# Kernel tuning notes

Measured on AMD Instinct MI355X. Metric: run time of the kernel, lower is better.

The kernel has to match this reference:

```python
import jax, jax.numpy as jnp
import numpy as np

IN_F = 512
OUT_F = 512
ALPHA = 0.1  # leaky relu slope
NEG_INF = jnp.float32(-9e15)


def setup_inputs() -> dict:
    key = jax.random.key(0)
    k1, k2, k3, k4, k5 = jax.random.split(key, 5)
    bs, t = 16, 1024
    x_a = jax.random.normal(k1, (bs, t, IN_F), dtype=jnp.float32)
    x_v = jax.random.normal(k2, (bs, t, IN_F), dtype=jnp.float32)
    adj = jax.random.randint(k3, (bs, 2 * t, 2 * t), 0, 2, dtype=jnp.int32)
    # xavier_uniform with gain=1.414
    gain = 1.414
    limW = gain * np.sqrt(6.0 / (IN_F + OUT_F))
    W = jax.random.uniform(k4, (IN_F, OUT_F), minval=-limW, maxval=limW, dtype=jnp.float32)
    lima = gain * np.sqrt(6.0 / (2 * OUT_F + 1))
    a = jax.random.uniform(k5, (2 * OUT_F, 1), minval=-lima, maxval=lima, dtype=jnp.float32)
    return {"x_a": x_a, "x_v": x_v, "adj": adj, "W": W, "a": a}


def reference(x_a, x_v, adj, W, a):
    # h: (bs, 2t, in_f)
    h = jnp.concatenate([x_a, x_v], axis=1)
    Wh = jnp.matmul(h, W)                      # (bs, 2t, out_f)
    Wh1 = jnp.matmul(Wh, a[:OUT_F, :])         # (bs, 2t, 1)
    Wh2 = jnp.matmul(Wh, a[OUT_F:, :])         # (bs, 2t, 1)
    e = jax.nn.leaky_relu(Wh1 + jnp.swapaxes(Wh2, -1, -2), negative_slope=ALPHA)  # (bs, 2t, 2t)
    attention = jnp.where(adj > 0, e, NEG_INF)
    attention = jax.nn.softmax(attention, axis=-1)
    h_prime = jnp.matmul(attention, Wh)        # (bs, 2t, out_f)
    h_prime = jax.nn.elu(h_prime)
    t = x_a.shape[1]
    return h_prime[:, :t, :], h_prime[:, t:, :]
```

## Files before the change

### kernel.cpp

```cpp
#include <hip/hip_runtime.h>
#include <hip/hip_bf16.h>
#include <stdint.h>

typedef __attribute__((ext_vector_type(4))) float f32x4;
typedef __attribute__((ext_vector_type(8))) short short8;
typedef __attribute__((ext_vector_type(8))) unsigned short u16x8;
typedef __attribute__((ext_vector_type(4))) unsigned short u16x4;

typedef __attribute__((address_space(1))) const unsigned int as1_u32;
typedef __attribute__((address_space(3))) unsigned int as3_u32;
#define GLD16(src, dst) __builtin_amdgcn_global_load_lds((as1_u32*)(src), (as3_u32*)(dst), 16, 0, 0)

__device__ __forceinline__ unsigned short f2bf(float f) {
  unsigned int u = __float_as_uint(f);
  u += 0x7fffu + ((u >> 16) & 1u);
  return (unsigned short)(u >> 16);
}
__device__ __forceinline__ float bf2f(unsigned short h) {
  return __uint_as_float(((unsigned int)h) << 16);
}

__global__ __launch_bounds__(256) void k_twp(const float* __restrict__ W,
                                             unsigned short* __restrict__ WT) {
  __shared__ float tile[64][65];
  int tid = threadIdx.x;
  int c = tid & 63, r0 = tid >> 6;
  int kb = blockIdx.x * 64, nb = blockIdx.y * 64;
#pragma unroll
  for (int rr = 0; rr < 16; ++rr) {
    int r = rr * 4 + r0;
    tile[r][c] = W[(size_t)(kb + r) * 512 + nb + c];
  }
  __syncthreads();
#pragma unroll
  for (int rr = 0; rr < 16; ++rr) {
    int r = rr * 4 + r0;
    WT[(size_t)(nb + r) * 512 + kb + c] = f2bf(tile[c][r]);
  }
}

__global__ __launch_bounds__(256, 2) void k_gemm(const float* __restrict__ xa,
                                                 const float* __restrict__ xv,
                                                 const unsigned short* __restrict__ WT,
                                                 unsigned short* __restrict__ WhT) {
  __shared__ __align__(16) unsigned short Al[64 * 64];
  __shared__ __align__(16) unsigned short Bl[512 * 64];
  int tid = threadIdx.x;
  int rblk = blockIdx.x;
  int R0g = rblk * 64;
  int b = R0g >> 11;
  int iloc = R0g & 2047;
  const float* Abase = (iloc < 1024)
      ? (xa + ((size_t)b * 1024 + iloc) * 512)
      : (xv + ((size_t)b * 1024 + (iloc - 1024)) * 512);

  int lane = tid & 63;
  int wid = tid >> 6;
  int wc = wid;

  f32x4 acc[4][8];
#pragma unroll
  for (int i = 0; i < 4; ++i)
#pragma unroll
    for (int j = 0; j < 8; ++j) acc[i][j] = (f32x4){0.f, 0.f, 0.f, 0.f};

  for (int kt = 0; kt < 8; ++kt) {
    int k0 = kt * 64;
    __syncthreads();
#pragma unroll
    for (int pass = 0; pass < 4; ++pass) {
      int row = pass * 16 + (tid >> 4);
      int gg = tid & 15;
      float4 v = *((const float4*)(Abase + (size_t)row * 512 + k0) + gg);
      u16x4 pk;
      pk.x = f2bf(v.x); pk.y = f2bf(v.y); pk.z = f2bf(v.z); pk.w = f2bf(v.w);
      *(u16x4*)((char*)Al + row * 128 + ((gg * 8) ^ ((row & 7) << 4))) = pk;
    }
#pragma unroll
    for (int pass = 0; pass < 16; ++pass) {
      int n = pass * 32 + (tid >> 3);
      int g = tid & 7;
      const unsigned short* src = WT + (size_t)n * 512 + k0 + ((g ^ (n & 7)) << 3);
      unsigned short* dst = Bl + pass * 2048 + wid * 512;
      GLD16(src, dst);
    }
    __syncthreads();
#pragma unroll
    for (int kc = 0; kc < 2; ++kc) {
      int u = kc * 4 + (lane >> 4);
      short8 af[4];
#pragma unroll
      for (int mf = 0; mf < 4; ++mf) {
        int row = mf * 16 + (lane & 15);
        af[mf] = *(const short8*)((const char*)Al + row * 128 + (((u ^ (row & 7)) & 7) << 4));
      }
#pragma unroll
      for (int nf = 0; nf < 8; ++nf) {
        int n = wc * 128 + nf * 16 + (lane & 15);
        short8 bv = *(const short8*)((const char*)Bl + n * 128 + (((u ^ (n & 7)) & 7) << 4));
#pragma unroll
        for (int mf = 0; mf < 4; ++mf)
          acc[mf][nf] = __builtin_amdgcn_mfma_f32_16x16x32_bf16(af[mf], bv, acc[mf][nf], 0, 0, 0);
      }
    }
  }
#pragma unroll
  for (int mf = 0; mf < 4; ++mf) {
    int jrow = iloc + mf * 16 + ((lane >> 4) << 2);
#pragma unroll
    for (int nf = 0; nf < 8; ++nf) {
      int n = wc * 128 + nf * 16 + (lane & 15);
      u16x4 pk;
#pragma unroll
      for (int e = 0; e < 4; ++e) pk[e] = f2bf(acc[mf][nf][e]);
      *(u16x4*)(WhT + ((size_t)b * 512 + n) * 2048 + jrow) = pk;
    }
  }
}

__global__ __launch_bounds__(256) void k_s(const unsigned short* __restrict__ WhT,
                                           const float* __restrict__ a,
                                           float* __restrict__ s1, float* __restrict__ s2,
                                           float* __restrict__ f1, float* __restrict__ f2) {
  __shared__ float a1l[512], a2l[512];
  __shared__ float S1p[8][256], S2p[8][256];
  int tid = threadIdx.x;
  int b = blockIdx.y;
  int j0 = blockIdx.x * 256;
  a1l[tid] = a[tid]; a1l[256 + tid] = a[256 + tid];
  a2l[tid] = a[512 + tid]; a2l[256 + tid] = a[768 + tid];
  __syncthreads();
  int jv = (tid & 31) * 8;
  int nh = tid >> 5;
  const unsigned short* base = WhT + ((size_t)b * 512 + nh * 64) * 2048 + j0 + jv;
  float c1[8], c2[8];
#pragma unroll
  for (int e = 0; e < 8; ++e) { c1[e] = 0.f; c2[e] = 0.f; }
#pragma unroll 4
  for (int i = 0; i < 64; ++i) {
    u16x8 w = *(const u16x8*)(base + (size_t)i * 2048);
    float w1 = a1l[nh * 64 + i], w2 = a2l[nh * 64 + i];
#pragma unroll
    for (int e = 0; e < 8; ++e) {
      float wv = bf2f(w[e]);
      c1[e] += wv * w1;
      c2[e] += wv * w2;
    }
  }
#pragma unroll
  for (int e = 0; e < 8; ++e) { S1p[nh][jv + e] = c1[e]; S2p[nh][jv + e] = c2[e]; }
  __syncthreads();
  float v1 = 0.f, v2 = 0.f;
#pragma unroll
  for (int h = 0; h < 8; ++h) { v1 += S1p[h][tid]; v2 += S2p[h][tid]; }
  size_t o = (size_t)b * 2048 + j0 + tid;
  s1[o] = v1; s2[o] = v2;
  f1[o] = __expf(v2);
  f2[o] = __expf(0.1f * v2);
}

__global__ __launch_bounds__(512, 2) void k_attn(const int* __restrict__ adj,
                                                 const unsigned short* __restrict__ WhT,
                                                 const float* __restrict__ s1g,
                                                 const float* __restrict__ s2g,
                                                 const float* __restrict__ f1g,
                                                 const float* __restrict__ f2g,
                                                 float* __restrict__ out) {
  __shared__ __align__(16) unsigned short Bl[2 * 512 * 32];
  __shared__ __align__(16) unsigned short Pl[2 * 128 * 32];
  __shared__ float f1l[2048], f2l[2048];
  __shared__ float zl[128];
  __shared__ float red[8];
  int tid = threadIdx.x;
  int bx = blockIdx.x;
  int q = bx >> 3, xcd = bx & 7;
  int b = xcd * 2 + (q & 1);
  int rb = q >> 1;
  int R0 = rb * 128;

  int lane = tid & 63, wid = tid >> 6;
  int wr2 = wid >> 2, wc = wid & 3;
  int r = tid >> 2, qc = tid & 3;

  const unsigned short* whbase = WhT + (size_t)b * 512 * 2048;
  const int* adjrow = adj + ((size_t)b * 2048 + R0 + r) * 2048 + qc * 8;

  auto stageB = [&](int j0h, int buf) {
#pragma unroll
    for (int pass = 0; pass < 4; ++pass) {
      int n = pass * 128 + (tid >> 2);
      int g = tid & 3;
      const unsigned short* src = whbase + (size_t)n * 2048 + j0h + ((g ^ (n & 3)) << 3);
      unsigned short* dst = Bl + buf * 16384 + pass * 4096 + wid * 512;
      GLD16(src, dst);
    }
  };

  stageB(0, 0);
  int4 aL0 = *(const int4*)(adjrow + 0);
  int4 aL1 = *(const int4*)(adjrow + 4);
  int4 aH0 = *(const int4*)(adjrow + 32);
  int4 aH1 = *(const int4*)(adjrow + 36);

  float lm = -1e30f;
#pragma unroll
  for (int i = 0; i < 4; ++i) {
    int idx = i * 512 + tid;
    float v = s2g[(size_t)b * 2048 + idx];
    f1l[idx] = f1g[(size_t)b * 2048 + idx];
    f2l[idx] = f2g[(size_t)b * 2048 + idx];
    lm = fmaxf(lm, v);
  }
#pragma unroll
  for (int s = 1; s < 64; s <<= 1) lm = fmaxf(lm, __shfl_xor(lm, s));
  if (lane == 0) red[wid] = lm;
  __syncthreads();
  float gmax = red[0];
#pragma unroll
  for (int i = 1; i < 8; ++i) gmax = fmaxf(gmax, red[i]);

  float s1r = s1g[(size_t)b * 2048 + R0 + r];
  float t0v = s1r + gmax;
  float M = (t0v > 0.f) ? t0v : 0.1f * t0v;
  float E1 = __expf(s1r - M);
  float E2 = __expf(0.1f * s1r - M);
  float T1 = __expf(-s1r);
  float zacc = 0.f;

  f32x4 acc[4][8];
#pragma unroll
  for (int i = 0; i < 4; ++i)
#pragma unroll
    for (int j = 0; j < 8; ++j) acc[i][j] = (f32x4){0.f, 0.f, 0.f, 0.f};

  auto computeP = [&](int j0h, int buf, int4 a0, int4 a1) {
    int av[8];
    av[0] = a0.x; av[1] = a0.y; av[2] = a0.z; av[3] = a0.w;
    av[4] = a1.x; av[5] = a1.y; av[6] = a1.z; av[7] = a1.w;
    int jb = j0h + qc * 8;
    float4 A1 = *(const float4*)(f1l + jb);
    float4 B1 = *(const float4*)(f1l + jb + 4);
    float4 A2 = *(const float4*)(f2l + jb);
    float4 B2 = *(const float4*)(f2l + jb + 4);
    float f1v[8] = {A1.x, A1.y, A1.z, A1.w, B1.x, B1.y, B1.z, B1.w};
    float f2v[8] = {A2.x, A2.y, A2.z, A2.w, B2.x, B2.y, B2.z, B2.w};
    u16x8 pk;
#pragma unroll
    for (int c = 0; c < 8; ++c) {
      bool pos = f1v[c] > T1;
      float Ev = pos ? E1 : E2;
      float Fv = pos ? f1v[c] : f2v[c];
      float p = (av[c] > 0) ? Ev * Fv : 0.f;
      unsigned short pb = f2bf(p);
      zacc += bf2f(pb);
      pk[c] = pb;
    }
    *(u16x8*)((char*)(Pl + buf * 4096) + r * 64 + ((qc ^ (r & 3)) << 4)) = pk;
  };

  auto mfmaPhase = [&](int buf) {
    const char* pb = (const char*)(Pl + buf * 4096);
    const char* bb = (const char*)(Bl + buf * 16384);
    int u = lane >> 4;
    short8 af[4];
#pragma unroll
    for (int mf = 0; mf < 4; ++mf) {
      int row = wr2 * 64 + mf * 16 + (lane & 15);
      af[mf] = *(const short8*)(pb + row * 64 + ((u ^ (row & 3)) << 4));
    }
#pragma unroll
    for (int nf = 0; nf < 8; ++nf) {
      int n = wc * 128 + nf * 16 + (lane & 15);
      short8 bv = *(const short8*)(bb + n * 64 + ((u ^ (n & 3)) << 4));
#pragma unroll
      for (int mf = 0; mf < 4; ++mf)
        acc[mf][nf] = __builtin_amdgcn_mfma_f32_16x16x32_bf16(af[mf], bv, acc[mf][nf], 0, 0, 0);
    }
  };

  __syncthreads();
  computeP(0, 0, aL0, aL1);
  __syncthreads();

  int4 aHn0 = aH0, aHn1 = aH1, aLn0 = aL0, aLn1 = aL1;
  for (int t = 0; t < 32; ++t) {
    int j0 = t << 6;
    if (t < 31) {
      aLn0 = *(const int4*)(adjrow + j0 + 64);
      aLn1 = *(const int4*)(adjrow + j0 + 68);
      aHn0 = *(const int4*)(adjrow + j0 + 96);
      aHn1 = *(const int4*)(adjrow + j0 + 100);
    }
    stageB(j0 + 32, 1);
    computeP(j0 + 32, 1, aH0, aH1);
    mfmaPhase(0);
    __syncthreads();
    if (t < 31) {
      stageB(j0 + 64, 0);
      computeP(j0 + 64, 0, aLn0, aLn1);
    }
    mfmaPhase(1);
    __syncthreads();
    aH0 = aHn0; aH1 = aHn1;
  }

  zacc += __shfl_xor(zacc, 1);
  zacc += __shfl_xor(zacc, 2);
  if (qc == 0) zl[r] = zacc;
  __syncthreads();

  float* obase;
  if (R0 < 1024) obase = out + ((size_t)b * 1024 + R0) * 512;
  else obase = out + (size_t)8388608 + ((size_t)b * 1024 + (R0 - 1024)) * 512;
#pragma unroll
  for (int mf = 0; mf < 4; ++mf) {
    int row0 = wr2 * 64 + mf * 16 + ((lane >> 4) << 2);
    float zi[4];
#pragma unroll
    for (int e = 0; e < 4; ++e) zi[e] = 1.f / zl[row0 + e];
#pragma unroll
    for (int nf = 0; nf < 8; ++nf) {
      int n = wc * 128 + nf * 16 + (lane & 15);
#pragma unroll
      for (int e = 0; e < 4; ++e) {
        float v = acc[mf][nf][e] * zi[e];
        v = (v > 0.f) ? v : (__expf(v) - 1.f);
        obase[(size_t)(row0 + e) * 512 + n] = v;
      }
    }
  }
}

extern "C" void kernel_launch(void* const* d_in, const int* in_sizes, int n_in,
                              void* d_out, int out_size, void* d_ws, size_t ws_size,
                              hipStream_t stream) {
  (void)in_sizes; (void)n_in; (void)out_size; (void)ws_size;
  const float* x_a = (const float*)d_in[0];
  const float* x_v = (const float*)d_in[1];
  const int*   adj = (const int*)d_in[2];
  const float* W   = (const float*)d_in[3];
  const float* a   = (const float*)d_in[4];
  float* out = (float*)d_out;

  char* ws = (char*)d_ws;
  unsigned short* WT  = (unsigned short*)ws;
  unsigned short* WhT = (unsigned short*)(ws + (1u << 19));
  float* s1 = (float*)(ws + (1u << 19) + (1u << 25));
  float* s2 = s1 + 32768;
  float* f1 = s2 + 32768;
  float* f2 = f1 + 32768;

  hipLaunchKernelGGL(k_twp,  dim3(8, 8),   dim3(256), 0, stream, W, WT);
  hipLaunchKernelGGL(k_gemm, dim3(512),    dim3(256), 0, stream, x_a, x_v, WT, WhT);
  hipLaunchKernelGGL(k_s,    dim3(8, 16),  dim3(256), 0, stream, WhT, a, s1, s2, f1, f2);
  hipLaunchKernelGGL(k_attn, dim3(256),    dim3(512), 0, stream, adj, WhT, s1, s2, f1, f2, out);
}
```

Baseline: 498.3 us.

## Fuse score projection into GEMM epilogue and stage adjacency via async LDS loads

The separate k_s kernel is removed. The attention score vectors s1/s2 and their exponentials are now computed in the GEMM epilogue from the fp32 accumulators, using shuffle and LDS reductions. This saves a kernel launch and a re-read of WhT. In the attention kernel, adjacency tiles are prefetched into LDS with global_load_lds alongside the WhT tiles, replacing register prefetch. The loop is restructured into 64 single-buffered phases with explicit vmcnt/lgkmcnt waits and raw barriers. This adds LDS usage and relies on hand-tuned waitcnt counts being correct.

```diff
diff --git a/kernel.cpp b/kernel.cpp
--- a/kernel.cpp
+++ b/kernel.cpp
@@ -42,9 +42,14 @@
 __global__ __launch_bounds__(256, 2) void k_gemm(const float* __restrict__ xa,
                                                  const float* __restrict__ xv,
                                                  const unsigned short* __restrict__ WT,
-                                                 unsigned short* __restrict__ WhT) {
+                                                 unsigned short* __restrict__ WhT,
+                                                 const float* __restrict__ a,
+                                                 float* __restrict__ s1, float* __restrict__ s2,
+                                                 float* __restrict__ f1, float* __restrict__ f2) {
   __shared__ __align__(16) unsigned short Al[64 * 64];
   __shared__ __align__(16) unsigned short Bl[512 * 64];
+  __shared__ float a1l[512], a2l[512];
+  __shared__ float sp1[4][64], sp2[4][64];
   int tid = threadIdx.x;
   int rblk = blockIdx.x;
   int R0g = rblk * 64;
@@ -58,6 +63,12 @@
   int wid = tid >> 6;
   int wc = wid;
 
+#pragma unroll
+  for (int i = 0; i < 2; ++i) {
+    a1l[i * 256 + tid] = a[i * 256 + tid];
+    a2l[i * 256 + tid] = a[512 + i * 256 + tid];
+  }
+
   f32x4 acc[4][8];
 #pragma unroll
   for (int i = 0; i < 4; ++i)
@@ -104,6 +115,7 @@
       }
     }
   }
+
 #pragma unroll
   for (int mf = 0; mf < 4; ++mf) {
     int jrow = iloc + mf * 16 + ((lane >> 4) << 2);
@@ -116,47 +128,54 @@
       *(u16x4*)(WhT + ((size_t)b * 512 + n) * 2048 + jrow) = pk;
     }
   }
-}
-
-__global__ __launch_bounds__(256) void k_s(const unsigned short* __restrict__ WhT,
-                                           const float* __restrict__ a,
-                                           float* __restrict__ s1, float* __restrict__ s2,
-                                           float* __restrict__ f1, float* __restrict__ f2) {
-  __shared__ float a1l[512], a2l[512];
-  __shared__ float S1p[8][256], S2p[8][256];
-  int tid = threadIdx.x;
-  int b = blockIdx.y;
-  int j0 = blockIdx.x * 256;
-  a1l[tid] = a[tid]; a1l[256 + tid] = a[256 + tid];
-  a2l[tid] = a[512 + tid]; a2l[256 + tid] = a[768 + tid];
+
+  float p1[4][4], p2[4][4];
+#pragma unroll
+  for (int mf = 0; mf < 4; ++mf)
+#pragma unroll
+    for (int e = 0; e < 4; ++e) { p1[mf][e] = 0.f; p2[mf][e] = 0.f; }
+#pragma unroll
+  for (int nf = 0; nf < 8; ++nf) {
+    int n = wc * 128 + nf * 16 + (lane & 15);
+    float w1 = a1l[n], w2 = a2l[n];
+#pragma unroll
+    for (int mf = 0; mf < 4; ++mf)
+#pragma unroll
+      for (int e = 0; e < 4; ++e) {
+        p1[mf][e] += acc[mf][nf][e] * w1;
+        p2[mf][e] += acc[mf][nf][e] * w2;
+      }
+  }
+#pragma unroll
+  for (int mask = 1; mask < 16; mask <<= 1) {
+#pragma unroll
+    for (int mf = 0; mf < 4; ++mf)
+#pragma unroll
+      for (int e = 0; e < 4; ++e) {
+        p1[mf][e] += __shfl_xor(p1[mf][e], mask);
+        p2[mf][e] += __shfl_xor(p2[mf][e], mask);
+      }
+  }
+  if ((lane & 15) == 0) {
+    int u = lane >> 4;
+#pragma unroll
+    for (int mf = 0; mf < 4; ++mf)
+#pragma unroll
+      for (int e = 0; e < 4; ++e) {
+        int jl = mf * 16 + u * 4 + e;
+        sp1[wc][jl] = p1[mf][e];
+        sp2[wc][jl] = p2[mf][e];
+      }
+  }
   __syncthreads();
-  int jv = (tid & 31) * 8;
-  int nh = tid >> 5;
-  const unsigned short* base = WhT + ((size_t)b * 512 + nh * 64) * 2048 + j0 + jv;
-  float c1[8], c2[8];
-#pragma unroll
-  for (int e = 0; e < 8; ++e) { c1[e] = 0.f; c2[e] = 0.f; }
-#pragma unroll 4
-  for (int i = 0; i < 64; ++i) {
-    u16x8 w = *(const u16x8*)(base + (size_t)i * 2048);
-    float w1 = a1l[nh * 64 + i], w2 = a2l[nh * 64 + i];
-#pragma unroll
-    for (int e = 0; e < 8; ++e) {
-      float wv = bf2f(w[e]);
-      c1[e] += wv * w1;
-      c2[e] += wv * w2;
-    }
-  }
-#pragma unroll
-  for (int e = 0; e < 8; ++e) { S1p[nh][jv + e] = c1[e]; S2p[nh][jv + e] = c2[e]; }
-  __syncthreads();
-  float v1 = 0.f, v2 = 0.f;
-#pragma unroll
-  for (int h = 0; h < 8; ++h) { v1 += S1p[h][tid]; v2 += S2p[h][tid]; }
-  size_t o = (size_t)b * 2048 + j0 + tid;
-  s1[o] = v1; s2[o] = v2;
-  f1[o] = __expf(v2);
-  f2[o] = __expf(0.1f * v2);
+  if (tid < 64) {
+    float v1 = sp1[0][tid] + sp1[1][tid] + sp1[2][tid] + sp1[3][tid];
+    float v2 = sp2[0][tid] + sp2[1][tid] + sp2[2][tid] + sp2[3][tid];
+    size_t o = (size_t)b * 2048 + iloc + tid;
+    s1[o] = v1; s2[o] = v2;
+    f1[o] = __expf(v2);
+    f2[o] = __expf(0.1f * v2);
+  }
 }
 
 __global__ __launch_bounds__(512, 2) void k_attn(const int* __restrict__ adj,
@@ -166,8 +185,9 @@
                                                  const float* __restrict__ f1g,
                                                  const float* __restrict__ f2g,
                                                  float* __restrict__ out) {
-  __shared__ __align__(16) unsigned short Bl[2 * 512 * 32];
-  __shared__ __align__(16) unsigned short Pl[2 * 128 * 32];
+  __shared__ __align__(16) unsigned short Bl[2][512 * 32];
+  __shared__ __align__(16) int AdjL[2][128 * 32];
+  __shared__ __align__(16) unsigned short Pl[2][128 * 32];
   __shared__ float f1l[2048], f2l[2048];
   __shared__ float zl[128];
   __shared__ float red[8];
@@ -183,24 +203,28 @@
   int r = tid >> 2, qc = tid & 3;
 
   const unsigned short* whbase = WhT + (size_t)b * 512 * 2048;
-  const int* adjrow = adj + ((size_t)b * 2048 + R0 + r) * 2048 + qc * 8;
-
-  auto stageB = [&](int j0h, int buf) {
-#pragma unroll
-    for (int pass = 0; pass < 4; ++pass) {
-      int n = pass * 128 + (tid >> 2);
-      int g = tid & 3;
-      const unsigned short* src = whbase + (size_t)n * 2048 + j0h + ((g ^ (n & 3)) << 3);
-      unsigned short* dst = Bl + buf * 16384 + pass * 4096 + wid * 512;
-      GLD16(src, dst);
+  const int* adjbase = adj + ((size_t)b * 2048 + R0) * 2048;
+
+  auto issue = [&](int ph) {
+    int j0 = ph << 5;
+    int buf = ph & 1;
+#pragma unroll
+    for (int p = 0; p < 4; ++p) {
+      int G = p * 512 + tid;
+      int n = G >> 2, g = G & 3;
+      const unsigned short* src = whbase + (size_t)n * 2048 + j0 + ((g ^ (n & 3)) << 3);
+      GLD16(src, (unsigned short*)Bl[buf] + G * 8);
+    }
+#pragma unroll
+    for (int p = 0; p < 2; ++p) {
+      int G = p * 512 + tid;
+      int rr = G >> 3, g = G & 7;
+      const int* src = adjbase + (size_t)rr * 2048 + j0 + ((g ^ (rr & 7)) << 2);
+      GLD16(src, AdjL[buf] + G * 4);
     }
   };
 
-  stageB(0, 0);
-  int4 aL0 = *(const int4*)(adjrow + 0);
-  int4 aL1 = *(const int4*)(adjrow + 4);
-  int4 aH0 = *(const int4*)(adjrow + 32);
-  int4 aH1 = *(const int4*)(adjrow + 36);
+  issue(0);
 
   float lm = -1e30f;
 #pragma unroll
@@ -233,15 +257,16 @@
 #pragma unroll
     for (int j = 0; j < 8; ++j) acc[i][j] = (f32x4){0.f, 0.f, 0.f, 0.f};
 
-  auto computeP = [&](int j0h, int buf, int4 a0, int4 a1) {
-    int av[8];
-    av[0] = a0.x; av[1] = a0.y; av[2] = a0.z; av[3] = a0.w;
-    av[4] = a1.x; av[5] = a1.y; av[6] = a1.z; av[7] = a1.w;
-    int jb = j0h + qc * 8;
+  auto computeP = [&](int ph) {
+    int buf = ph & 1;
+    int jb = (ph << 5) + qc * 8;
+    int4 a0 = *(const int4*)(AdjL[buf] + r * 32 + (((qc * 2 + 0) ^ (r & 7)) << 2));
+    int4 a1 = *(const int4*)(AdjL[buf] + r * 32 + (((qc * 2 + 1) ^ (r & 7)) << 2));
     float4 A1 = *(const float4*)(f1l + jb);
     float4 B1 = *(const float4*)(f1l + jb + 4);
     float4 A2 = *(const float4*)(f2l + jb);
     float4 B2 = *(const float4*)(f2l + jb + 4);
+    int av[8] = {a0.x, a0.y, a0.z, a0.w, a1.x, a1.y, a1.z, a1.w};
     float f1v[8] = {A1.x, A1.y, A1.z, A1.w, B1.x, B1.y, B1.z, B1.w};
     float f2v[8] = {A2.x, A2.y, A2.z, A2.w, B2.x, B2.y, B2.z, B2.w};
     u16x8 pk;
@@ -255,53 +280,46 @@
       zacc += bf2f(pb);
       pk[c] = pb;
     }
-    *(u16x8*)((char*)(Pl + buf * 4096) + r * 64 + ((qc ^ (r & 3)) << 4)) = pk;
+    *(u16x8*)((char*)Pl[buf] + r * 64 + ((qc ^ (r & 3)) << 4)) = pk;
   };
 
-  auto mfmaPhase = [&](int buf) {
-    const char* pb = (const char*)(Pl + buf * 4096);
-    const char* bb = (const char*)(Bl + buf * 16384);
+  auto mfmaPhase = [&](int ph) {
+    int buf = ph & 1;
     int u = lane >> 4;
     short8 af[4];
 #pragma unroll
     for (int mf = 0; mf < 4; ++mf) {
       int row = wr2 * 64 + mf * 16 + (lane & 15);
-      af[mf] = *(const short8*)(pb + row * 64 + ((u ^ (row & 3)) << 4));
+      af[mf] = *(const short8*)((const char*)Pl[buf] + row * 64 + ((u ^ (row & 3)) << 4));
     }
 #pragma unroll
     for (int nf = 0; nf < 8; ++nf) {
       int n = wc * 128 + nf * 16 + (lane & 15);
-      short8 bv = *(const short8*)(bb + n * 64 + ((u ^ (n & 3)) << 4));
+      short8 bv = *(const short8*)((const char*)Bl[buf] + n * 64 + ((u ^ (n & 3)) << 4));
 #pragma unroll
       for (int mf = 0; mf < 4; ++mf)
         acc[mf][nf] = __builtin_amdgcn_mfma_f32_16x16x32_bf16(af[mf], bv, acc[mf][nf], 0, 0, 0);
     }
   };
 
-  __syncthreads();
-  computeP(0, 0, aL0, aL1);
-  __syncthreads();
-
-  int4 aHn0 = aH0, aHn1 = aH1, aLn0 = aL0, aLn1 = aL1;
-  for (int t = 0; t < 32; ++t) {
-    int j0 = t << 6;
-    if (t < 31) {
-      aLn0 = *(const int4*)(adjrow + j0 + 64);
-      aLn1 = *(const int4*)(adjrow + j0 + 68);
-      aHn0 = *(const int4*)(adjrow + j0 + 96);
-      aHn1 = *(const int4*)(adjrow + j0 + 100);
-    }
-    stageB(j0 + 32, 1);
-    computeP(j0 + 32, 1, aH0, aH1);
-    mfmaPhase(0);
-    __syncthreads();
-    if (t < 31) {
-      stageB(j0 + 64, 0);
-      computeP(j0 + 64, 0, aLn0, aLn1);
-    }
-    mfmaPhase(1);
-    __syncthreads();
-    aH0 = aHn0; aH1 = aHn1;
+  issue(1);
+  computeP(0);
+  asm volatile("s_waitcnt lgkmcnt(0)" ::: "memory");
+  __builtin_amdgcn_s_barrier();
+  mfmaPhase(0);
+
+  for (int ph = 1; ph < 64; ++ph) {
+    __builtin_amdgcn_s_barrier();
+    if (ph < 63) {
+      issue(ph + 1);
+      asm volatile("s_waitcnt vmcnt(6)" ::: "memory");
+    } else {
+      asm volatile("s_waitcnt vmcnt(0)" ::: "memory");
+    }
+    computeP(ph);
+    asm volatile("s_waitcnt lgkmcnt(0)" ::: "memory");
+    __builtin_amdgcn_s_barrier();
+    mfmaPhase(ph);
   }
 
   zacc += __shfl_xor(zacc, 1);
@@ -350,8 +368,7 @@
   float* f1 = s2 + 32768;
   float* f2 = f1 + 32768;
 
-  hipLaunchKernelGGL(k_twp,  dim3(8, 8),   dim3(256), 0, stream, W, WT);
-  hipLaunchKernelGGL(k_gemm, dim3(512),    dim3(256), 0, stream, x_a, x_v, WT, WhT);
-  hipLaunchKernelGGL(k_s,    dim3(8, 16),  dim3(256), 0, stream, WhT, a, s1, s2, f1, f2);
-  hipLaunchKernelGGL(k_attn, dim3(256),    dim3(512), 0, stream, adj, WhT, s1, s2, f1, f2, out);
-}
+  hipLaunchKernelGGL(k_twp,  dim3(8, 8), dim3(256), 0, stream, W, WT);
+  hipLaunchKernelGGL(k_gemm, dim3(512),  dim3(256), 0, stream, x_a, x_v, WT, WhT, a, s1, s2, f1, f2);
+  hipLaunchKernelGGL(k_attn, dim3(256),  dim3(512), 0, stream, adj, WhT, s1, s2, f1, f2, out);
+}
```

Result: slower. 510.3 us (+2.4%).
